# Performance work log

Hardware: AMD Instinct MI355X
Metric: run time of the kernel (lower is better)

## Reference

```python
import jax, jax.numpy as jnp
import numpy as np

NUM_IN_CH = 64
DIM = 256
HEADS = 8


def conv1x1(x, w):
    # x: [b,c,h,w], w: [o,c,1,1] -> [b,o,h,w]
    return jnp.einsum('bchw,oc->bohw', x, w[:, :, 0, 0])


def dwconv3(x, w):
    # depthwise 3x3, padding=1; w: [c,1,3,3]
    return jax.lax.conv_general_dilated(
        x, w, window_strides=(1, 1), padding='SAME',
        feature_group_count=x.shape[1],
        dimension_numbers=('NCHW', 'OIHW', 'NCHW'))


def setup_inputs() -> dict:
    key = jax.random.key(0)
    ks = jax.random.split(key, 12)
    B, C, H, W = 8, NUM_IN_CH, 128, 128
    s = 0.02
    return {
        'x': jax.random.normal(ks[0], (B, C, H, W), jnp.float32),
        'y': jax.random.normal(ks[1], (B, C, H, W), jnp.float32),
        'z': jax.random.normal(ks[2], (B, C, H, W), jnp.float32),
        'Wq': jax.random.normal(ks[3], (DIM, C, 1, 1), jnp.float32) * s,
        'Wq_dw': jax.random.normal(ks[4], (DIM, 1, 3, 3), jnp.float32) * s,
        'Wk': jax.random.normal(ks[5], (DIM, C, 1, 1), jnp.float32) * s,
        'Wk_dw': jax.random.normal(ks[6], (DIM, 1, 3, 3), jnp.float32) * s,
        'Wv': jax.random.normal(ks[7], (DIM, C, 1, 1), jnp.float32) * s,
        'Wv_dw': jax.random.normal(ks[8], (DIM, 1, 3, 3), jnp.float32) * s,
        'Wproj': jax.random.normal(ks[9], (DIM, DIM, 1, 1), jnp.float32) * s,
        'Wfus': jax.random.normal(ks[10], (DIM, 3 * C, 1, 1), jnp.float32) * s,
        'temperature': jnp.ones((HEADS, 1, 1), jnp.float32),
    }


def reference(x, y, z, Wq, Wq_dw, Wk, Wk_dw, Wv, Wv_dw, Wproj, Wfus, temperature):
    b, c, h, w = x.shape
    hw = h * w
    q = dwconv3(conv1x1(x, Wq), Wq_dw)
    k = dwconv3(conv1x1(y, Wk), Wk_dw)
    v = dwconv3(conv1x1(z, Wv), Wv_dw)
    f = conv1x1(jnp.concatenate([x, y, z], axis=1), Wfus)

    def to_heads(t):  # [b, dim, h, w] -> [b, head, c_head, hw]
        return t.reshape(b, HEADS, DIM // HEADS, hw)

    q, k, v = to_heads(q), to_heads(k), to_heads(v)
    # L2-normalize over the spatial (hw) axis, eps matches torch F.normalize
    qn = q / jnp.maximum(jnp.sqrt(jnp.sum(q * q, axis=-1, keepdims=True)), 1e-12)
    kn = k / jnp.maximum(jnp.sqrt(jnp.sum(k * k, axis=-1, keepdims=True)), 1e-12)
    attn = jnp.einsum('bhcn,bhdn->bhcd', qn, kn) * temperature  # [b,head,c,c]
    attn = jax.nn.softmax(attn, axis=-1)
    out = jnp.einsum('bhcd,bhdn->bhcn', attn, v).reshape(b, DIM, h, w)
    out = conv1x1(out, Wproj)
    return out + f
```

## Files before the change

kernel.cpp:

```cpp
#include <hip/hip_runtime.h>
#include <cstdint>

#define B_   8
#define CIN  64
#define DIM_ 256
#define H_   128
#define W_   128
#define HW_  (H_*W_)

typedef unsigned short u16;
typedef unsigned int   u32;
typedef short short8 __attribute__((ext_vector_type(8)));
typedef float f32x4  __attribute__((ext_vector_type(4)));

__device__ __forceinline__ u16 f2bf(float f) {
    u32 u = __float_as_uint(f);
    u32 r = (u + 0x7fffu + ((u >> 16) & 1u)) >> 16;
    return (u16)r;
}
__device__ __forceinline__ float bf2f(u16 h) {
    return __uint_as_float(((u32)h) << 16);
}

__global__ __launch_bounds__(256) void conv_mfma_kernel(
    const float* __restrict__ in, const float* __restrict__ Wc,
    u16* __restrict__ pre)
{
    __shared__ u16 Alds[256 * 64];
    __shared__ u16 Blds[128 * 64];

    const int tid = threadIdx.x;
    const int b = blockIdx.y;
    const int px0 = blockIdx.x * 128;

    {
        const int row = tid;
        const float* wp = Wc + (size_t)row * 64;
        #pragma unroll
        for (int s = 0; s < 8; ++s) {
            float4 f0 = *(const float4*)(wp + s * 8);
            float4 f1 = *(const float4*)(wp + s * 8 + 4);
            uint4 pk;
            pk.x = f2bf(f0.x) | ((u32)f2bf(f0.y) << 16);
            pk.y = f2bf(f0.z) | ((u32)f2bf(f0.w) << 16);
            pk.z = f2bf(f1.x) | ((u32)f2bf(f1.y) << 16);
            pk.w = f2bf(f1.z) | ((u32)f2bf(f1.w) << 16);
            *(uint4*)&Alds[row * 64 + ((s * 8) ^ ((row & 7) << 3))] = pk;
        }
    }
    #pragma unroll
    for (int v4 = 0; v4 < 4; ++v4) {
        int it = tid + v4 * 256;
        int px = it & 127, cg = it >> 7;
        const float* sp = in + ((size_t)b * CIN + cg * 8) * HW_ + px0 + px;
        u32 wv[4];
        #pragma unroll
        for (int j = 0; j < 4; ++j) {
            float a = sp[(size_t)(2 * j) * HW_];
            float c = sp[(size_t)(2 * j + 1) * HW_];
            wv[j] = f2bf(a) | ((u32)f2bf(c) << 16);
        }
        *(uint4*)&Blds[px * 64 + ((cg * 8) ^ ((px & 7) << 3))] =
            make_uint4(wv[0], wv[1], wv[2], wv[3]);
    }
    __syncthreads();

    const int lane = tid & 63, wid = tid >> 6;
    const int g = lane >> 4, ln = lane & 15;
    const int m0 = wid * 64;
    f32x4 acc[4][8] = {};

    #pragma unroll
    for (int ks = 0; ks < 2; ++ks) {
        short8 af[4];
        #pragma unroll
        for (int fm = 0; fm < 4; ++fm) {
            int m = m0 + fm * 16 + ln;
            af[fm] = *(const short8*)&Alds[m * 64 + ((ks * 32 + g * 8) ^ ((m & 7) << 3))];
        }
        #pragma unroll
        for (int fn = 0; fn < 8; ++fn) {
            int p = fn * 16 + ln;
            short8 bf = *(const short8*)&Blds[p * 64 + ((ks * 32 + g * 8) ^ ((p & 7) << 3))];
            #pragma unroll
            for (int fm = 0; fm < 4; ++fm)
                acc[fm][fn] = __builtin_amdgcn_mfma_f32_16x16x32_bf16(af[fm], bf, acc[fm][fn], 0, 0, 0);
        }
    }

    u16* op = pre + (size_t)b * DIM_ * HW_;
    #pragma unroll
    for (int fm = 0; fm < 4; ++fm)
        #pragma unroll
        for (int fn = 0; fn < 8; ++fn)
            #pragma unroll
            for (int r = 0; r < 4; ++r) {
                int ch = m0 + fm * 16 + g * 4 + r;
                op[(size_t)ch * HW_ + px0 + fn * 16 + ln] = f2bf(acc[fm][fn][r]);
            }
}

__global__ __launch_bounds__(256) void dw_kernel(
    const u16* __restrict__ pre, const float* __restrict__ Wd,
    u16* __restrict__ dst)
{
    __shared__ u16 t0[34][144];

    const int tid = threadIdx.x;
    const int y0 = blockIdx.x * 32;
    const int ch = blockIdx.y;
    const int b = blockIdx.z;
    const u16* src = pre + ((size_t)b * DIM_ + ch) * HW_;

    for (int i = tid; i < 68; i += 256)
        t0[i >> 1][(i & 1) ? 136 : 7] = 0;
    for (int i = tid; i < 544; i += 256) {
        int row = i >> 4, seg = i & 15;
        int gy = y0 - 1 + row;
        uint4 v = make_uint4(0, 0, 0, 0);
        if (gy >= 0 && gy < H_) v = *(const uint4*)(src + (size_t)gy * W_ + seg * 8);
        *(uint4*)&t0[row][8 + seg * 8] = v;
    }
    const float* wv = Wd + (size_t)ch * 9;
    float w00 = wv[0], w01 = wv[1], w02 = wv[2];
    float w10 = wv[3], w11 = wv[4], w12 = wv[5];
    float w20 = wv[6], w21 = wv[7], w22 = wv[8];
    __syncthreads();

    const int px = tid & 127, half = tid >> 7;
    u16* op = dst + ((size_t)b * DIM_ + ch) * HW_;
    float h0m2 = 0.f, h0m1 = 0.f, h1m1 = 0.f;
    #pragma unroll
    for (int y = 0; y < 18; ++y) {
        int r = half * 16 + y;
        float v0 = bf2f(t0[r][7 + px]);
        float v1 = bf2f(t0[r][8 + px]);
        float v2 = bf2f(t0[r][9 + px]);
        float h0 = fmaf(v0, w00, fmaf(v1, w01, v2 * w02));
        float h1 = fmaf(v0, w10, fmaf(v1, w11, v2 * w12));
        float h2 = fmaf(v0, w20, fmaf(v1, w21, v2 * w22));
        if (y >= 2)
            op[(size_t)(y0 + half * 16 + y - 2) * W_ + px] = f2bf(h0m2 + h1m1 + h2);
        h0m2 = h0m1; h0m1 = h0; h1m1 = h1;
    }
}

__global__ __launch_bounds__(256) void gram_mfma_kernel(
    const u16* __restrict__ q, const u16* __restrict__ k,
    float* __restrict__ pgram, float* __restrict__ pssq, float* __restrict__ pssk)
{
    __shared__ float red[4][1024];
    __shared__ float redq[4][32];
    __shared__ float redk[4][32];

    const int bh = blockIdx.y;
    const int chunk = blockIdx.x;
    const int tid = threadIdx.x;
    const int lane = tid & 63, wid = tid >> 6;
    const int g = lane >> 4, ln = lane & 15;

    const size_t off = (size_t)(bh * 32 + ln) * HW_ + chunk * 2048 + wid * 512 + g * 8;
    const u16* qp = q + off;
    const u16* kp = k + off;

    f32x4 aqk[2][2] = {};
    f32x4 aqq[2] = {};
    f32x4 akk[2] = {};

    #pragma unroll 4
    for (int n = 0; n < 512; n += 32) {
        short8 qf[2], kf[2];
        qf[0] = *(const short8*)(qp + n);
        qf[1] = *(const short8*)(qp + (size_t)16 * HW_ + n);
        kf[0] = *(const short8*)(kp + n);
        kf[1] = *(const short8*)(kp + (size_t)16 * HW_ + n);
        #pragma unroll
        for (int ti = 0; ti < 2; ++ti)
            #pragma unroll
            for (int tj = 0; tj < 2; ++tj)
                aqk[ti][tj] = __builtin_amdgcn_mfma_f32_16x16x32_bf16(qf[ti], kf[tj], aqk[ti][tj], 0, 0, 0);
        #pragma unroll
        for (int ti = 0; ti < 2; ++ti) {
            aqq[ti] = __builtin_amdgcn_mfma_f32_16x16x32_bf16(qf[ti], qf[ti], aqq[ti], 0, 0, 0);
            akk[ti] = __builtin_amdgcn_mfma_f32_16x16x32_bf16(kf[ti], kf[ti], akk[ti], 0, 0, 0);
        }
    }

    #pragma unroll
    for (int ti = 0; ti < 2; ++ti)
        #pragma unroll
        for (int tj = 0; tj < 2; ++tj)
            #pragma unroll
            for (int r = 0; r < 4; ++r)
                red[wid][(ti * 16 + g * 4 + r) * 32 + tj * 16 + ln] = aqk[ti][tj][r];
    if ((ln >> 2) == g) {
        #pragma unroll
        for (int ti = 0; ti < 2; ++ti) {
            redq[wid][ti * 16 + ln] = aqq[ti][ln & 3];
            redk[wid][ti * 16 + ln] = akk[ti][ln & 3];
        }
    }
    __syncthreads();

    for (int p = tid; p < 1024; p += 256) {
        float s = red[0][p] + red[1][p] + red[2][p] + red[3][p];
        pgram[((size_t)bh * 8 + chunk) * 1024 + p] = s;
    }
    if (tid < 32) {
        pssq[((size_t)bh * 8 + chunk) * 32 + tid] =
            redq[0][tid] + redq[1][tid] + redq[2][tid] + redq[3][tid];
    } else if (tid < 64) {
        int j = tid & 31;
        pssk[((size_t)bh * 8 + chunk) * 32 + j] =
            redk[0][j] + redk[1][j] + redk[2][j] + redk[3][j];
    }
}

__global__ __launch_bounds__(256) void softproj_kernel(
    const float* __restrict__ pgram, const float* __restrict__ pssq,
    const float* __restrict__ pssk, const float* __restrict__ Wproj,
    const float* __restrict__ temp, u16* __restrict__ Amm)
{
    __shared__ float att[32][33];
    __shared__ float nq[32], nk[32];

    const int bh = blockIdx.x;
    const int h = bh & 7;
    const int b = bh >> 3;
    const int tid = threadIdx.x;

    for (int p = tid; p < 1024; p += 256) {
        float s = 0.f;
        #pragma unroll
        for (int c = 0; c < 8; ++c) s += pgram[((size_t)bh * 8 + c) * 1024 + p];
        att[p >> 5][p & 31] = s;
    }
    if (tid < 32) {
        float s = 0.f;
        #pragma unroll
        for (int c = 0; c < 8; ++c) s += pssq[((size_t)bh * 8 + c) * 32 + tid];
        nq[tid] = fmaxf(sqrtf(s), 1e-12f);
    } else if (tid < 64) {
        int i = tid & 31;
        float s = 0.f;
        #pragma unroll
        for (int c = 0; c < 8; ++c) s += pssk[((size_t)bh * 8 + c) * 32 + i];
        nk[i] = fmaxf(sqrtf(s), 1e-12f);
    }
    __syncthreads();

    const float T = temp[h];
    if (tid < 32) {
        int i = tid;
        float row[32];
        float mx = -1e30f;
        float qi = T / nq[i];
        #pragma unroll
        for (int j = 0; j < 32; ++j) {
            float v = att[i][j] * qi / nk[j];
            row[j] = v;
            mx = fmaxf(mx, v);
        }
        float s = 0.f;
        #pragma unroll
        for (int j = 0; j < 32; ++j) { float e = expf(row[j] - mx); row[j] = e; s += e; }
        float inv = 1.f / s;
        #pragma unroll
        for (int j = 0; j < 32; ++j) att[i][j] = row[j] * inv;
    }
    __syncthreads();

    const int o = tid;
    float wp[32];
    #pragma unroll
    for (int i2 = 0; i2 < 32; i2 += 4)
        *(float4*)&wp[i2] = *(const float4*)&Wproj[(size_t)o * DIM_ + h * 32 + i2];
    u16* arow = Amm + ((size_t)b * DIM_ + o) * DIM_ + h * 32;
    #pragma unroll
    for (int j = 0; j < 32; ++j) {
        float s = 0.f;
        #pragma unroll
        for (int i = 0; i < 32; ++i) s = fmaf(wp[i], att[i][j], s);
        arow[j] = f2bf(s);
    }
}

__global__ __launch_bounds__(256) void wfus_cast_kernel(
    const float* __restrict__ Wfus, u16* __restrict__ Afus)
{
    int idx = blockIdx.x * 256 + threadIdx.x;
    int base = idx * 8;
    float4 f0 = *(const float4*)(Wfus + base);
    float4 f1 = *(const float4*)(Wfus + base + 4);
    uint4 pk;
    pk.x = f2bf(f0.x) | ((u32)f2bf(f0.y) << 16);
    pk.y = f2bf(f0.z) | ((u32)f2bf(f0.w) << 16);
    pk.z = f2bf(f1.x) | ((u32)f2bf(f1.y) << 16);
    pk.w = f2bf(f1.z) | ((u32)f2bf(f1.w) << 16);
    *(uint4*)(Afus + base) = pk;
}

#define LOADB_F4(KC, W) do {                                                    \
    if ((KC) < 4) {                                                             \
        _Pragma("unroll") for (int i_ = 0; i_ < 2; ++i_) {                      \
            const u16* vb_ = vbuf + ((size_t)b * DIM_ + (KC) * 64 + (qq0 + 2 * i_) * 16) * HW_ + px0 + pxu; \
            _Pragma("unroll") for (int jj_ = 0; jj_ < 8; ++jj_)                 \
                W[i_][jj_] = (u32)vb_[(size_t)(2 * jj_) * HW_]                  \
                           | ((u32)vb_[(size_t)(2 * jj_ + 1) * HW_] << 16);     \
        }                                                                       \
    } else {                                                                    \
        const float* bp_ = ((KC) == 4) ? xin : ((KC) == 5) ? yin : zin;         \
        _Pragma("unroll") for (int i_ = 0; i_ < 2; ++i_) {                      \
            const float* sp_ = bp_ + ((size_t)b * CIN + (qq0 + 2 * i_) * 16) * HW_ + px0 + pxu; \
            _Pragma("unroll") for (int jj_ = 0; jj_ < 8; ++jj_)                 \
                W[i_][jj_] = (u32)f2bf(sp_[(size_t)(2 * jj_) * HW_])            \
                           | ((u32)f2bf(sp_[(size_t)(2 * jj_ + 1) * HW_]) << 16); \
        }                                                                       \
    } } while (0)

#define WRITEB_F4(BUF, W) do {                                                  \
    u16* dd_ = &Bl[BUF][pxu * 64];                                              \
    _Pragma("unroll") for (int i_ = 0; i_ < 2; ++i_) {                          \
        int qq_ = qq0 + 2 * i_;                                                 \
        *(uint4*)&dd_[(qq_ * 16)     ^ ((pxu & 7) << 3)] = make_uint4(W[i_][0], W[i_][1], W[i_][2], W[i_][3]); \
        *(uint4*)&dd_[(qq_ * 16 + 8) ^ ((pxu & 7) << 3)] = make_uint4(W[i_][4], W[i_][5], W[i_][6], W[i_][7]); \
    } } while (0)

#define LOADA_F4(KC, A) do {                                                    \
    _Pragma("unroll") for (int ks_ = 0; ks_ < 2; ++ks_)                         \
    _Pragma("unroll") for (int fm_ = 0; fm_ < 2; ++fm_) {                       \
        int m_ = m0 + fm_ * 16 + ln;                                            \
        const u16* ap_ = ((KC) < 4)                                             \
            ? Amm + ((size_t)b * DIM_ + m_) * DIM_ + (KC) * 64 + ks_ * 32 + g * 8 \
            : Afus + (size_t)m_ * 192 + ((KC) - 4) * 64 + ks_ * 32 + g * 8;     \
        A[ks_ * 2 + fm_] = *(const short8*)ap_;                                 \
    } } while (0)

__global__ __launch_bounds__(256, 4) void final4_kernel(
    const u16* __restrict__ Amm, const u16* __restrict__ Afus,
    const u16* __restrict__ vbuf,
    const float* __restrict__ xin, const float* __restrict__ yin,
    const float* __restrict__ zin, float* __restrict__ out)
{
    __shared__ u16 Bl[2][128 * 64];

    const int tid = threadIdx.x;
    const int px0 = blockIdx.x * 128;
    const int o0  = blockIdx.y * 128;
    const int b   = blockIdx.z;
    const int lane = tid & 63, wid = tid >> 6;
    const int g = lane >> 4, ln = lane & 15;
    const int m0 = o0 + wid * 32;
    const int pxu = tid & 127;
    const int qq0 = tid >> 7;

    f32x4 acc[2][8] = {};
    short8 aC[4], aN[4];
    u32 wN[2][8];

    LOADA_F4(0, aC);
    {
        u32 w0[2][8];
        LOADB_F4(0, w0);
        WRITEB_F4(0, w0);
    }
    __syncthreads();
    LOADA_F4(1, aN);
    LOADB_F4(1, wN);

    #pragma unroll
    for (int kc = 0; kc < 7; ++kc) {
        const int cur = kc & 1;

        #pragma unroll
        for (int ks = 0; ks < 2; ++ks)
            #pragma unroll
            for (int fn = 0; fn < 8; ++fn) {
                int p = fn * 16 + ln;
                short8 bf = *(const short8*)&Bl[cur][p * 64 + ((ks * 32 + g * 8) ^ ((p & 7) << 3))];
                acc[0][fn] = __builtin_amdgcn_mfma_f32_16x16x32_bf16(aC[ks * 2 + 0], bf, acc[0][fn], 0, 0, 0);
                acc[1][fn] = __builtin_amdgcn_mfma_f32_16x16x32_bf16(aC[ks * 2 + 1], bf, acc[1][fn], 0, 0, 0);
            }

        if (kc < 6) {
            WRITEB_F4(cur ^ 1, wN);
            __syncthreads();
            #pragma unroll
            for (int r = 0; r < 4; ++r) aC[r] = aN[r];
            if (kc < 5) {
                LOADA_F4(kc + 2, aN);
                LOADB_F4(kc + 2, wN);
            }
        }
    }

    float* op = out + (size_t)b * DIM_ * HW_;
    #pragma unroll
    for (int fm = 0; fm < 2; ++fm)
        #pragma unroll
        for (int fn = 0; fn < 8; ++fn)
            #pragma unroll
            for (int r = 0; r < 4; ++r) {
                int ch = m0 + fm * 16 + g * 4 + r;
                op[(size_t)ch * HW_ + px0 + fn * 16 + ln] = acc[fm][fn][r];
            }
}

extern "C" void kernel_launch(void* const* d_in, const int* in_sizes, int n_in,
                              void* d_out, int out_size, void* d_ws, size_t ws_size,
                              hipStream_t stream) {
    (void)in_sizes; (void)n_in; (void)out_size; (void)ws_size;

    const float* x     = (const float*)d_in[0];
    const float* y     = (const float*)d_in[1];
    const float* z     = (const float*)d_in[2];
    const float* Wq    = (const float*)d_in[3];
    const float* Wqd   = (const float*)d_in[4];
    const float* Wk    = (const float*)d_in[5];
    const float* Wkd   = (const float*)d_in[6];
    const float* Wv    = (const float*)d_in[7];
    const float* Wvd   = (const float*)d_in[8];
    const float* Wproj = (const float*)d_in[9];
    const float* Wfus  = (const float*)d_in[10];
    const float* temp  = (const float*)d_in[11];

    const size_t QELEMS = (size_t)B_ * DIM_ * HW_;

    u16* preb = (u16*)d_out;
    u16* qbuf = (u16*)d_out + QELEMS;
    u16* kvbuf = (u16*)d_ws;
    char* wsp = (char*)d_ws + QELEMS * sizeof(u16);
    float* pgram = (float*)wsp;                       wsp += 64 * 8 * 1024 * 4;
    float* pssq  = (float*)wsp;                       wsp += 64 * 8 * 32 * 4;
    float* pssk  = (float*)wsp;                       wsp += 64 * 8 * 32 * 4;
    u16*   Amm   = (u16*)wsp;                         wsp += (size_t)B_ * DIM_ * DIM_ * 2;
    u16*   Afus  = (u16*)wsp;

    dim3 cgrid(128, B_);
    dim3 dgrid(4, DIM_, B_);

    wfus_cast_kernel<<<24, 256, 0, stream>>>(Wfus, Afus);
    conv_mfma_kernel<<<cgrid, 256, 0, stream>>>(x, Wq, preb);
    dw_kernel<<<dgrid, 256, 0, stream>>>(preb, Wqd, qbuf);
    conv_mfma_kernel<<<cgrid, 256, 0, stream>>>(y, Wk, preb);
    dw_kernel<<<dgrid, 256, 0, stream>>>(preb, Wkd, kvbuf);
    gram_mfma_kernel<<<dim3(8, 64), 256, 0, stream>>>(qbuf, kvbuf, pgram, pssq, pssk);
    softproj_kernel<<<64, 256, 0, stream>>>(pgram, pssq, pssk, Wproj, temp, Amm);
    conv_mfma_kernel<<<cgrid, 256, 0, stream>>>(z, Wv, preb);
    dw_kernel<<<dgrid, 256, 0, stream>>>(preb, Wvd, kvbuf);
    final4_kernel<<<dim3(128, 2, B_), 256, 0, stream>>>(Amm, Afus, kvbuf, x, y, z, (float*)d_out);
}
```

Before: 300.9 us.

## Fuse 1x1 conv and depthwise 3x3 into one halo-tiled kernel

Merges the pointwise MFMA convolution with the depthwise 3x3 conv. Each block computes a 16x16 spatial tile plus a 1-pixel halo (18x18) for all 256 channels, keeps the intermediate in LDS, and applies the depthwise stencil in place. This removes the bf16 round trip of the pre-activation tensor through global memory and halves kernel launches. In exchange it recomputes the halo pixels, uses large LDS per block (limiting occupancy), and writes output in 16-pixel strided rows, which is less coalesced.

Measured after the change: 277.5 us. 1.08x faster.

```diff
diff --git a/kernel.cpp b/kernel.cpp
--- a/kernel.cpp
+++ b/kernel.cpp
@@ -22,22 +22,26 @@
     return __uint_as_float(((u32)h) << 16);
 }
 
-__global__ __launch_bounds__(256) void conv_mfma_kernel(
+__global__ __launch_bounds__(512) void convdw_kernel(
     const float* __restrict__ in, const float* __restrict__ Wc,
-    u16* __restrict__ pre)
+    const float* __restrict__ Wd, u16* __restrict__ dst)
 {
-    __shared__ u16 Alds[256 * 64];
-    __shared__ u16 Blds[128 * 64];
+    __shared__ u16 Wt[256 * 64];
+    __shared__ u16 Xt[336 * 64];
+    __shared__ u16 Pt[64 * 340];
+    __shared__ float wlds[9 * 68];
 
     const int tid = threadIdx.x;
+    const int tile = blockIdx.x;
     const int b = blockIdx.y;
-    const int px0 = blockIdx.x * 128;
+    const int y0 = (tile >> 3) * 16;
+    const int x0 = (tile & 7) * 16;
 
     {
-        const int row = tid;
-        const float* wp = Wc + (size_t)row * 64;
-        #pragma unroll
-        for (int s = 0; s < 8; ++s) {
+        const int row = tid >> 1, hh = tid & 1;
+        const float* wp = Wc + (size_t)row * 64 + hh * 32;
+        #pragma unroll
+        for (int s = 0; s < 4; ++s) {
             float4 f0 = *(const float4*)(wp + s * 8);
             float4 f1 = *(const float4*)(wp + s * 8 + 4);
             uint4 pk;
@@ -45,103 +49,108 @@
             pk.y = f2bf(f0.z) | ((u32)f2bf(f0.w) << 16);
             pk.z = f2bf(f1.x) | ((u32)f2bf(f1.y) << 16);
             pk.w = f2bf(f1.z) | ((u32)f2bf(f1.w) << 16);
-            *(uint4*)&Alds[row * 64 + ((s * 8) ^ ((row & 7) << 3))] = pk;
-        }
-    }
-    #pragma unroll
-    for (int v4 = 0; v4 < 4; ++v4) {
-        int it = tid + v4 * 256;
-        int px = it & 127, cg = it >> 7;
-        const float* sp = in + ((size_t)b * CIN + cg * 8) * HW_ + px0 + px;
-        u32 wv[4];
-        #pragma unroll
-        for (int j = 0; j < 4; ++j) {
-            float a = sp[(size_t)(2 * j) * HW_];
-            float c = sp[(size_t)(2 * j + 1) * HW_];
-            wv[j] = f2bf(a) | ((u32)f2bf(c) << 16);
-        }
-        *(uint4*)&Blds[px * 64 + ((cg * 8) ^ ((px & 7) << 3))] =
-            make_uint4(wv[0], wv[1], wv[2], wv[3]);
+            int o = hh * 32 + s * 8;
+            *(uint4*)&Wt[row * 64 + (o ^ ((row & 7) << 3))] = pk;
+        }
+    }
+    {
+        const float* inb = in + (size_t)b * CIN * HW_;
+        for (int i = tid; i < 2592; i += 512) {
+            int chg = i / 324;
+            int px = i - chg * 324;
+            int py = px / 18;
+            int pxi = px - py * 18;
+            int gy = y0 - 1 + py, gx = x0 - 1 + pxi;
+            uint4 pk = make_uint4(0, 0, 0, 0);
+            if (gy >= 0 && gy < H_ && gx >= 0 && gx < W_) {
+                const float* sp = inb + (size_t)(chg * 8) * HW_ + (size_t)gy * W_ + gx;
+                u32 wv[4];
+                #pragma unroll
+                for (int j = 0; j < 4; ++j) {
+                    float a = sp[(size_t)(2 * j) * HW_];
+                    float c = sp[(size_t)(2 * j + 1) * HW_];
+                    wv[j] = f2bf(a) | ((u32)f2bf(c) << 16);
+                }
+                pk = make_uint4(wv[0], wv[1], wv[2], wv[3]);
+            }
+            *(uint4*)&Xt[px * 64 + ((chg * 8) ^ ((px & 7) << 3))] = pk;
+        }
     }
     __syncthreads();
 
-    const int lane = tid & 63, wid = tid >> 6;
+    const int lane = tid & 63, w = tid >> 6;
     const int g = lane >> 4, ln = lane & 15;
-    const int m0 = wid * 64;
-    f32x4 acc[4][8] = {};
-
-    #pragma unroll
-    for (int ks = 0; ks < 2; ++ks) {
-        short8 af[4];
-        #pragma unroll
-        for (int fm = 0; fm < 4; ++fm) {
-            int m = m0 + fm * 16 + ln;
-            af[fm] = *(const short8*)&Alds[m * 64 + ((ks * 32 + g * 8) ^ ((m & 7) << 3))];
-        }
-        #pragma unroll
-        for (int fn = 0; fn < 8; ++fn) {
-            int p = fn * 16 + ln;
-            short8 bf = *(const short8*)&Blds[p * 64 + ((ks * 32 + g * 8) ^ ((p & 7) << 3))];
-            #pragma unroll
-            for (int fm = 0; fm < 4; ++fm)
-                acc[fm][fn] = __builtin_amdgcn_mfma_f32_16x16x32_bf16(af[fm], bf, acc[fm][fn], 0, 0, 0);
-        }
-    }
-
-    u16* op = pre + (size_t)b * DIM_ * HW_;
-    #pragma unroll
-    for (int fm = 0; fm < 4; ++fm)
-        #pragma unroll
-        for (int fn = 0; fn < 8; ++fn)
-            #pragma unroll
-            for (int r = 0; r < 4; ++r) {
-                int ch = m0 + fm * 16 + g * 4 + r;
-                op[(size_t)ch * HW_ + px0 + fn * 16 + ln] = f2bf(acc[fm][fn][r]);
-            }
-}
-
-__global__ __launch_bounds__(256) void dw_kernel(
-    const u16* __restrict__ pre, const float* __restrict__ Wd,
-    u16* __restrict__ dst)
-{
-    __shared__ u16 t0[34][144];
-
-    const int tid = threadIdx.x;
-    const int y0 = blockIdx.x * 32;
-    const int ch = blockIdx.y;
-    const int b = blockIdx.z;
-    const u16* src = pre + ((size_t)b * DIM_ + ch) * HW_;
-
-    for (int i = tid; i < 68; i += 256)
-        t0[i >> 1][(i & 1) ? 136 : 7] = 0;
-    for (int i = tid; i < 544; i += 256) {
-        int row = i >> 4, seg = i & 15;
-        int gy = y0 - 1 + row;
-        uint4 v = make_uint4(0, 0, 0, 0);
-        if (gy >= 0 && gy < H_) v = *(const uint4*)(src + (size_t)gy * W_ + seg * 8);
-        *(uint4*)&t0[row][8 + seg * 8] = v;
-    }
-    const float* wv = Wd + (size_t)ch * 9;
-    float w00 = wv[0], w01 = wv[1], w02 = wv[2];
-    float w10 = wv[3], w11 = wv[4], w12 = wv[5];
-    float w20 = wv[6], w21 = wv[7], w22 = wv[8];
-    __syncthreads();
-
-    const int px = tid & 127, half = tid >> 7;
-    u16* op = dst + ((size_t)b * DIM_ + ch) * HW_;
-    float h0m2 = 0.f, h0m1 = 0.f, h1m1 = 0.f;
-    #pragma unroll
-    for (int y = 0; y < 18; ++y) {
-        int r = half * 16 + y;
-        float v0 = bf2f(t0[r][7 + px]);
-        float v1 = bf2f(t0[r][8 + px]);
-        float v2 = bf2f(t0[r][9 + px]);
-        float h0 = fmaf(v0, w00, fmaf(v1, w01, v2 * w02));
-        float h1 = fmaf(v0, w10, fmaf(v1, w11, v2 * w12));
-        float h2 = fmaf(v0, w20, fmaf(v1, w21, v2 * w22));
-        if (y >= 2)
-            op[(size_t)(y0 + half * 16 + y - 2) * W_ + px] = f2bf(h0m2 + h1m1 + h2);
-        h0m2 = h0m1; h0m1 = h0; h1m1 = h1;
+    const int wm = w & 3;
+    const int wpar = w >> 2;
+
+    u16* db = dst + (size_t)b * DIM_ * HW_;
+
+    for (int c = 0; c < 4; ++c) {
+        f32x4 acc[11];
+        #pragma unroll
+        for (int jj = 0; jj < 11; ++jj) acc[jj] = (f32x4){0.f, 0.f, 0.f, 0.f};
+        short8 af[2];
+        {
+            int m = c * 64 + wm * 16 + ln;
+            af[0] = *(const short8*)&Wt[m * 64 + ((g * 8) ^ ((m & 7) << 3))];
+            af[1] = *(const short8*)&Wt[m * 64 + ((32 + g * 8) ^ ((m & 7) << 3))];
+        }
+        #pragma unroll
+        for (int jj = 0; jj < 11; ++jj) {
+            int j = jj * 2 + wpar;
+            if (j < 21) {
+                int px = j * 16 + ln;
+                #pragma unroll
+                for (int ks = 0; ks < 2; ++ks) {
+                    short8 bf = *(const short8*)&Xt[px * 64 + ((ks * 32 + g * 8) ^ ((px & 7) << 3))];
+                    acc[jj] = __builtin_amdgcn_mfma_f32_16x16x32_bf16(af[ks], bf, acc[jj], 0, 0, 0);
+                }
+            }
+        }
+
+        if (c > 0) __syncthreads();
+
+        #pragma unroll
+        for (int jj = 0; jj < 11; ++jj) {
+            int j = jj * 2 + wpar;
+            if (j < 21) {
+                int px = j * 16 + ln;
+                #pragma unroll
+                for (int r = 0; r < 4; ++r)
+                    Pt[(wm * 16 + g * 4 + r) * 340 + px] = f2bf(acc[jj][r]);
+            }
+        }
+        for (int i = tid; i < 576; i += 512) {
+            int ch = i / 9, tap = i - ch * 9;
+            wlds[tap * 68 + ch] = Wd[(size_t)(c * 64 + ch) * 9 + tap];
+        }
+        __syncthreads();
+
+        #pragma unroll
+        for (int round = 0; round < 2; ++round) {
+            int item = tid + round * 512;
+            int chl = item >> 4, ox = item & 15;
+            float w00 = wlds[0 * 68 + chl], w01 = wlds[1 * 68 + chl], w02 = wlds[2 * 68 + chl];
+            float w10 = wlds[3 * 68 + chl], w11 = wlds[4 * 68 + chl], w12 = wlds[5 * 68 + chl];
+            float w20 = wlds[6 * 68 + chl], w21 = wlds[7 * 68 + chl], w22 = wlds[8 * 68 + chl];
+            const u16* prow = &Pt[chl * 340];
+            u16* op = db + (size_t)(c * 64 + chl) * HW_ + x0 + ox;
+            float h0m2 = 0.f, h0m1 = 0.f, h1m1 = 0.f;
+            #pragma unroll
+            for (int hy = 0; hy < 18; ++hy) {
+                float v0 = bf2f(prow[hy * 18 + ox]);
+                float v1 = bf2f(prow[hy * 18 + ox + 1]);
+                float v2 = bf2f(prow[hy * 18 + ox + 2]);
+                float h0 = fmaf(v0, w00, fmaf(v1, w01, v2 * w02));
+                float h1 = fmaf(v0, w10, fmaf(v1, w11, v2 * w12));
+                float h2 = fmaf(v0, w20, fmaf(v1, w21, v2 * w22));
+                if (hy >= 2)
+                    op[(size_t)(y0 + hy - 2) * W_] = f2bf(h0m2 + h1m1 + h2);
+                h0m2 = h0m1; h0m1 = h0; h1m1 = h1;
+            }
+        }
+        if (c == 3) break;
+        __syncthreads();
     }
 }
 
@@ -426,7 +435,6 @@
 
     const size_t QELEMS = (size_t)B_ * DIM_ * HW_;
 
-    u16* preb = (u16*)d_out;
     u16* qbuf = (u16*)d_out + QELEMS;
     u16* kvbuf = (u16*)d_ws;
     char* wsp = (char*)d_ws + QELEMS * sizeof(u16);
@@ -436,17 +444,13 @@
     u16*   Amm   = (u16*)wsp;                         wsp += (size_t)B_ * DIM_ * DIM_ * 2;
     u16*   Afus  = (u16*)wsp;
 
-    dim3 cgrid(128, B_);
-    dim3 dgrid(4, DIM_, B_);
+    dim3 fgrid(64, B_);
 
     wfus_cast_kernel<<<24, 256, 0, stream>>>(Wfus, Afus);
-    conv_mfma_kernel<<<cgrid, 256, 0, stream>>>(x, Wq, preb);
-    dw_kernel<<<dgrid, 256, 0, stream>>>(preb, Wqd, qbuf);
-    conv_mfma_kernel<<<cgrid, 256, 0, stream>>>(y, Wk, preb);
-    dw_kernel<<<dgrid, 256, 0, stream>>>(preb, Wkd, kvbuf);
+    convdw_kernel<<<fgrid, 512, 0, stream>>>(x, Wq, Wqd, qbuf);
+    convdw_kernel<<<fgrid, 512, 0, stream>>>(y, Wk, Wkd, kvbuf);
     gram_mfma_kernel<<<dim3(8, 64), 256, 0, stream>>>(qbuf, kvbuf, pgram, pssq, pssk);
     softproj_kernel<<<64, 256, 0, stream>>>(pgram, pssq, pssk, Wproj, temp, Amm);
-    conv_mfma_kernel<<<cgrid, 256, 0, stream>>>(z, Wv, preb);
-    dw_kernel<<<dgrid, 256, 0, stream>>>(preb, Wvd, kvbuf);
+    convdw_kernel<<<fgrid, 512, 0, stream>>>(z, Wv, Wvd, kvbuf);
     final4_kernel<<<dim3(128, 2, B_), 256, 0, stream>>>(Amm, Afus, kvbuf, x, y, z, (float*)d_out);
 }
```
